# Performance work log

Hardware: AMD Instinct MI355X
Metric: run time of the kernel (lower is better)

Reference implementation:

```python
import jax, jax.numpy as jnp
import numpy as np

N_DIMS = 64
N_HALF = N_DIMS // 2
HIDDEN = 512
N_LAYERS = 8
BATCH = 16384

IDX_EVEN = np.arange(0, N_DIMS, 2)  # mask != 0 for even layers
IDX_ODD = np.arange(1, N_DIMS, 2)


def _init_mlp_params(key, n_in, n_hidden, n_out, n_layers):
    ks = jax.random.split(key, 3)
    def lin(k, fi, fo):
        return jax.random.normal(k, (n_layers, fi, fo), dtype=jnp.float32) / np.sqrt(fi)
    W1 = lin(ks[0], n_in, n_hidden)
    W2 = lin(ks[1], n_hidden, n_hidden)
    W3 = lin(ks[2], n_hidden, n_out)
    b1 = jnp.zeros((n_layers, n_hidden), jnp.float32)
    b2 = jnp.zeros((n_layers, n_hidden), jnp.float32)
    b3 = jnp.zeros((n_layers, n_out), jnp.float32)
    return W1, b1, W2, b2, W3, b3


def setup_inputs() -> dict:
    key = jax.random.key(0)
    ky, kt, ks = jax.random.split(key, 3)
    y = jax.random.normal(ky, (BATCH, N_DIMS), dtype=jnp.float32)
    tW1, tb1, tW2, tb2, tW3, tb3 = _init_mlp_params(kt, N_HALF, HIDDEN, N_HALF, N_LAYERS)
    sW1, sb1, sW2, sb2, sW3, sb3 = _init_mlp_params(ks, N_HALF, HIDDEN, N_HALF, N_LAYERS)
    s_scale = jnp.ones((N_LAYERS, N_HALF), jnp.float32)
    s_shift = jnp.zeros((N_LAYERS, N_HALF), jnp.float32)
    return {
        "y": y,
        "tW1": tW1, "tb1": tb1, "tW2": tW2, "tb2": tb2, "tW3": tW3, "tb3": tb3,
        "sW1": sW1, "sb1": sb1, "sW2": sW2, "sb2": sb2, "sW3": sW3, "sb3": sb3,
        "s_scale": s_scale, "s_shift": s_shift,
    }


def _mlp(x, W1, b1, W2, b2, W3, b3):
    h = jax.nn.relu(x @ W1 + b1)
    h = jax.nn.relu(h @ W2 + b2)
    return h @ W3 + b3


def reference(y, tW1, tb1, tW2, tb2, tW3, tb3,
              sW1, sb1, sW2, sb2, sW3, sb3, s_scale, s_shift):
    z = y
    log_det = jnp.zeros_like(y)
    for i in range(N_LAYERS):
        i0 = IDX_EVEN if i % 2 == 0 else IDX_ODD  # transformed half
        i1 = IDX_ODD if i % 2 == 0 else IDX_EVEN  # conditioning half
        z0 = z[:, i0]  # [B, 32]
        z1 = z[:, i1]  # [B, 32]
        t = _mlp(z1, tW1[i], tb1[i], tW2[i], tb2[i], tW3[i], tb3[i])
        s = jnp.tanh(_mlp(z1, sW1[i], sb1[i], sW2[i], sb2[i], sW3[i], sb3[i])) * s_scale[i] + s_shift[i]
        z0 = z0 * jnp.exp(s) + t
        z = z.at[:, i0].set(z0)
        log_det = log_det.at[:, i0].add(s)
    return z, log_det
```

## Files before the change

kernel.cpp:

```cpp
#include <hip/hip_runtime.h>

typedef unsigned short u16;
typedef unsigned int   u32;
typedef _Float16 f16;
typedef __attribute__((ext_vector_type(8))) _Float16 half8;
typedef __attribute__((ext_vector_type(4))) float f32x4;

#define NBATCH 16384

__device__ __forceinline__ u16 f2h(float x) {
  union { f16 h; u16 u; } v; v.h = (f16)x; return v.u;
}

__global__ __launch_bounds__(256) void cvt_w(
    const float* __restrict__ tsrc, const float* __restrict__ ssrc,
    u16* __restrict__ dst, int M, int N)
{
  __shared__ float tile[32][33];
  int z = blockIdx.z;
  const float* src = ((z & 1) ? ssrc : tsrc) + (size_t)(z >> 1) * M * N;
  u16* d = dst + (size_t)z * M * N;
  int n0 = blockIdx.x * 32, m0 = blockIdx.y * 32;
  for (int r = 0; r < 4; r++) {
    int m = m0 + threadIdx.y + r * 8, n = n0 + threadIdx.x;
    tile[threadIdx.y + r * 8][threadIdx.x] = src[(size_t)m * N + n];
  }
  __syncthreads();
  for (int r = 0; r < 4; r++) {
    int n = n0 + threadIdx.y + r * 8, m = m0 + threadIdx.x;
    d[(size_t)n * M + m] = f2h(tile[threadIdx.x][threadIdx.y + r * 8]);
  }
}

__global__ __launch_bounds__(512, 2) void meganvp(
    const float* __restrict__ y,
    const u16* __restrict__ W1T, const u16* __restrict__ W2T, const u16* __restrict__ W3T,
    const float* __restrict__ tb1, const float* __restrict__ sb1,
    const float* __restrict__ tb2, const float* __restrict__ sb2,
    const float* __restrict__ tb3, const float* __restrict__ sb3,
    const float* __restrict__ s_scale, const float* __restrict__ s_shift,
    float* __restrict__ out)
{
  __shared__ u16 buf[64 * 512];
  __shared__ u16 X[64 * 40];
  __shared__ float TS[64 * 68];

  const int t = threadIdx.x;
  const int m0 = blockIdx.x * 64;
  const int lane = t & 63, w = t >> 6, lm = lane & 15, quad = lane >> 4;
  const int cw = w * 64;
  const int phase = blockIdx.x & 15;
  const int zr = t >> 3, zq = t & 7, c0 = zq * 8;

  float z[8], ld[8];
  {
    const float* yb = y + (size_t)(m0 + zr) * 64 + c0;
    f32x4 v0 = *(const f32x4*)&yb[0];
    f32x4 v1 = *(const f32x4*)&yb[4];
#pragma unroll
    for (int k = 0; k < 4; k++) { z[k] = v0[k]; z[4 + k] = v1[k]; }
#pragma unroll
    for (int e = 0; e < 8; e++) ld[e] = 0.f;
  }

  for (int layer = 0; layer < 8; layer++) {
    const int par = layer & 1;
    {
      union { u16 a[4]; uint2 v; } xv;
#pragma unroll
      for (int e = 0; e < 4; e++) xv.a[e] = f2h(z[2 * e + 1 - par]);
      *(uint2*)&X[zr * 40 + zq * 4] = xv.v;
    }
    __syncthreads();

    for (int net = 0; net < 2; net++) {
      const int idx = layer * 2 + net;

      {
        const float* b1p = (net ? sb1 : tb1) + layer * 512 + cw + lm;
        float bias1[4];
#pragma unroll
        for (int ct = 0; ct < 4; ct++) bias1[ct] = b1p[ct * 16];
        const u16* W1p = W1T + ((size_t)idx * 512 + cw + lm) * 32 + quad * 8;
        half8 bv[4];
#pragma unroll
        for (int ct = 0; ct < 4; ct++) bv[ct] = *(const half8*)&W1p[ct * 512];
        half8 av[4];
#pragma unroll
        for (int rt = 0; rt < 4; rt++)
          av[rt] = *(const half8*)&X[(rt * 16 + lm) * 40 + quad * 8];
        f32x4 zz = {0.f, 0.f, 0.f, 0.f};
        f32x4 acc[4][4];
#pragma unroll
        for (int rt = 0; rt < 4; rt++)
#pragma unroll
          for (int ct = 0; ct < 4; ct++)
            acc[rt][ct] = __builtin_amdgcn_mfma_f32_16x16x32_f16(av[rt], bv[ct], zz, 0, 0, 0);
#pragma unroll
        for (int rt = 0; rt < 4; rt++) {
          const int mrow = rt * 16 + quad * 4;
#pragma unroll
          for (int ct = 0; ct < 4; ct++) {
            const int n = cw + ct * 16 + lm;
#pragma unroll
            for (int r = 0; r < 4; r++) {
              float v = acc[rt][ct][r] + bias1[ct];
              v = v > 0.f ? v : 0.f;
              const int m = mrow + r;
              buf[m * 512 + ((((n >> 3) ^ (m & 7)) << 3) | (n & 7))] = f2h(v);
            }
          }
        }
      }
      __syncthreads();

      {
        const float* b2p = (net ? sb2 : tb2) + layer * 512 + cw + lm;
        float bias2[4];
#pragma unroll
        for (int ct = 0; ct < 4; ct++) bias2[ct] = b2p[ct * 16];
        const u16* W2p = W2T + ((size_t)idx * 512 + cw + lm) * 512 + quad * 8;
        f32x4 zz = {0.f, 0.f, 0.f, 0.f};
        f32x4 acc[4][4];
#pragma unroll
        for (int rt = 0; rt < 4; rt++)
#pragma unroll
          for (int ct = 0; ct < 4; ct++) acc[rt][ct] = zz;
        half8 bb[2][4];
        {
          const int kk0 = (phase & 15) * 32, kk1 = ((phase + 1) & 15) * 32;
#pragma unroll
          for (int ct = 0; ct < 4; ct++) {
            bb[0][ct] = *(const half8*)&W2p[ct * 8192 + kk0];
            bb[1][ct] = *(const half8*)&W2p[ct * 8192 + kk1];
          }
        }
#pragma unroll
        for (int ci = 0; ci < 16; ci++) {
          const int kk = ((ci + phase) & 15) * 32;
          half8 av[4];
#pragma unroll
          for (int rt = 0; rt < 4; rt++) {
            const int m = rt * 16 + lm;
            av[rt] = *(const half8*)&buf[m * 512 + ((((kk >> 3) + quad) ^ (m & 7)) << 3)];
          }
          half8 cur[4];
#pragma unroll
          for (int ct = 0; ct < 4; ct++) cur[ct] = bb[ci & 1][ct];
          if (ci < 14) {
            const int kn = ((ci + 2 + phase) & 15) * 32;
#pragma unroll
            for (int ct = 0; ct < 4; ct++)
              bb[ci & 1][ct] = *(const half8*)&W2p[ct * 8192 + kn];
          }
#pragma unroll
          for (int rt = 0; rt < 4; rt++)
#pragma unroll
            for (int ct = 0; ct < 4; ct++)
              acc[rt][ct] = __builtin_amdgcn_mfma_f32_16x16x32_f16(av[rt], cur[ct], acc[rt][ct], 0, 0, 0);
        }
        __syncthreads();
#pragma unroll
        for (int rt = 0; rt < 4; rt++) {
          const int mrow = rt * 16 + quad * 4;
#pragma unroll
          for (int ct = 0; ct < 4; ct++) {
            const int n = cw + ct * 16 + lm;
#pragma unroll
            for (int r = 0; r < 4; r++) {
              float v = acc[rt][ct][r] + bias2[ct];
              v = v > 0.f ? v : 0.f;
              const int m = mrow + r;
              buf[m * 512 + ((((n >> 3) ^ (m & 7)) << 3) | (n & 7))] = f2h(v);
            }
          }
        }
      }
      __syncthreads();

      {
        const int hr = (w & 3) * 16, hc = (w >> 2) * 16;
        const u16* W3p = W3T + ((size_t)idx * 32 + hc + lm) * 512 + quad * 8;
        f32x4 ha[2];
        ha[0] = (f32x4){0.f, 0.f, 0.f, 0.f}; ha[1] = ha[0];
        const int m = hr + lm;
#pragma unroll
        for (int ci = 0; ci < 16; ci++) {
          const int kk = ((ci + phase) & 15) * 32;
          half8 av = *(const half8*)&buf[m * 512 + ((((kk >> 3) + quad) ^ (m & 7)) << 3)];
          half8 bv = *(const half8*)&W3p[kk];
          ha[ci & 1] = __builtin_amdgcn_mfma_f32_16x16x32_f16(av, bv, ha[ci & 1], 0, 0, 0);
        }
        const int j = hc + lm;
        if (net == 0) {
          const float b3 = tb3[layer * 32 + j];
#pragma unroll
          for (int r = 0; r < 4; r++) {
            const int mm = hr + quad * 4 + r;
            TS[mm * 68 + 2 * j] = ha[0][r] + ha[1][r] + b3;
          }
        } else {
          const int jj = layer * 32 + j;
          const float b3 = sb3[jj], sc = s_scale[jj], sh = s_shift[jj];
#pragma unroll
          for (int r = 0; r < 4; r++) {
            const int mm = hr + quad * 4 + r;
            TS[mm * 68 + 2 * j + 1] = tanhf(ha[0][r] + ha[1][r] + b3) * sc + sh;
          }
        }
      }
      __syncthreads();
    }

    {
      const float* base = &TS[zr * 68 + zq * 8];
      f32x4 q0 = *(const f32x4*)&base[0];
      f32x4 q1 = *(const f32x4*)&base[4];
      float q[8];
#pragma unroll
      for (int k = 0; k < 4; k++) { q[k] = q0[k]; q[4 + k] = q1[k]; }
#pragma unroll
      for (int e = 0; e < 4; e++) {
        const float tv = q[2 * e], sv = q[2 * e + 1];
        const int zi = 2 * e + par;
        z[zi] = z[zi] * expf(sv) + tv;
        ld[zi] += sv;
      }
    }
    __syncthreads();
  }

  {
    float* zb = out + (size_t)(m0 + zr) * 64 + c0;
    float* lb = out + (size_t)NBATCH * 64 + (size_t)(m0 + zr) * 64 + c0;
    f32x4 v0, v1, l0, l1;
#pragma unroll
    for (int k = 0; k < 4; k++) {
      v0[k] = z[k]; v1[k] = z[4 + k];
      l0[k] = ld[k]; l1[k] = ld[4 + k];
    }
    *(f32x4*)&zb[0] = v0; *(f32x4*)&zb[4] = v1;
    *(f32x4*)&lb[0] = l0; *(f32x4*)&lb[4] = l1;
  }
}

extern "C" void kernel_launch(void* const* d_in, const int* in_sizes, int n_in,
                              void* d_out, int out_size, void* d_ws, size_t ws_size,
                              hipStream_t stream) {
  (void)in_sizes; (void)n_in; (void)out_size; (void)ws_size;
  const float* y   = (const float*)d_in[0];
  const float* tW1 = (const float*)d_in[1];
  const float* tb1 = (const float*)d_in[2];
  const float* tW2 = (const float*)d_in[3];
  const float* tb2 = (const float*)d_in[4];
  const float* tW3 = (const float*)d_in[5];
  const float* tb3 = (const float*)d_in[6];
  const float* sW1 = (const float*)d_in[7];
  const float* sb1 = (const float*)d_in[8];
  const float* sW2 = (const float*)d_in[9];
  const float* sb2 = (const float*)d_in[10];
  const float* sW3 = (const float*)d_in[11];
  const float* sb3 = (const float*)d_in[12];
  const float* s_scale = (const float*)d_in[13];
  const float* s_shift = (const float*)d_in[14];
  float* out = (float*)d_out;

  char* ws = (char*)d_ws;
  const size_t W1SZ = (size_t)16 * 512 * 32 * 2;
  const size_t W2SZ = (size_t)16 * 512 * 512 * 2;
  u16* W1 = (u16*)(ws);
  u16* W2 = (u16*)(ws + W1SZ);
  u16* W3 = (u16*)(ws + W1SZ + W2SZ);

  cvt_w<<<dim3(16, 1, 16), dim3(32, 8), 0, stream>>>(tW1, sW1, W1, 32, 512);
  cvt_w<<<dim3(16, 16, 16), dim3(32, 8), 0, stream>>>(tW2, sW2, W2, 512, 512);
  cvt_w<<<dim3(1, 16, 16), dim3(32, 8), 0, stream>>>(tW3, sW3, W3, 512, 32);

  meganvp<<<256, 512, 0, stream>>>(y, W1, W2, W3, tb1, sb1, tb2, sb2, tb3, sb3,
                                   s_scale, s_shift, out);
}
```

Baseline: 469.6 us.

## Double threads per block in coupling kernel and merge weight conversion launches

The fused coupling kernel now runs 1024 threads per block, so 16 waves split each 64-row tile into two 32-row halves while keeping a 64-column slice each. This halves per-wave accumulators and the register load, aiming for more waves in flight to hide MFMA and memory latency on the same 256 blocks. The three weight-conversion kernels are merged into one launch to cut launch overhead, and the trailing barrier after the z update is dropped. Every wave now loads the full W2 column slice for only half the rows, doubling W2 reads per block. Only half the waves work in the W3 stage, and launch_bounds(1024,4) may force tight register limits or spills.

```diff
diff --git a/kernel.cpp b/kernel.cpp
--- a/kernel.cpp
+++ b/kernel.cpp
@@ -12,15 +12,21 @@
   union { f16 h; u16 u; } v; v.h = (f16)x; return v.u;
 }
 
-__global__ __launch_bounds__(256) void cvt_w(
-    const float* __restrict__ tsrc, const float* __restrict__ ssrc,
-    u16* __restrict__ dst, int M, int N)
+__global__ __launch_bounds__(256) void cvt_all(
+    const float* __restrict__ tW1, const float* __restrict__ sW1,
+    const float* __restrict__ tW2, const float* __restrict__ sW2,
+    const float* __restrict__ tW3, const float* __restrict__ sW3,
+    u16* __restrict__ dW1, u16* __restrict__ dW2, u16* __restrict__ dW3)
 {
   __shared__ float tile[32][33];
-  int z = blockIdx.z;
+  const int z = blockIdx.z, bx = blockIdx.x;
+  const float *tsrc, *ssrc; u16* dst; int M, N, nt, mt;
+  if (bx < 16)       { tsrc = tW1; ssrc = sW1; dst = dW1; M = 32;  N = 512; nt = bx;           mt = 0; }
+  else if (bx < 272) { tsrc = tW2; ssrc = sW2; dst = dW2; M = 512; N = 512; nt = (bx - 16) & 15; mt = (bx - 16) >> 4; }
+  else               { tsrc = tW3; ssrc = sW3; dst = dW3; M = 512; N = 32;  nt = 0;            mt = bx - 272; }
   const float* src = ((z & 1) ? ssrc : tsrc) + (size_t)(z >> 1) * M * N;
   u16* d = dst + (size_t)z * M * N;
-  int n0 = blockIdx.x * 32, m0 = blockIdx.y * 32;
+  const int n0 = nt * 32, m0 = mt * 32;
   for (int r = 0; r < 4; r++) {
     int m = m0 + threadIdx.y + r * 8, n = n0 + threadIdx.x;
     tile[threadIdx.y + r * 8][threadIdx.x] = src[(size_t)m * N + n];
@@ -32,7 +38,7 @@
   }
 }
 
-__global__ __launch_bounds__(512, 2) void meganvp(
+__global__ __launch_bounds__(1024, 4) void meganvp(
     const float* __restrict__ y,
     const u16* __restrict__ W1T, const u16* __restrict__ W2T, const u16* __restrict__ W3T,
     const float* __restrict__ tb1, const float* __restrict__ sb1,
@@ -48,28 +54,26 @@
   const int t = threadIdx.x;
   const int m0 = blockIdx.x * 64;
   const int lane = t & 63, w = t >> 6, lm = lane & 15, quad = lane >> 4;
-  const int cw = w * 64;
+  const int r0 = (w & 1) * 32;
+  const int cw = (w >> 1) * 64;
   const int phase = blockIdx.x & 15;
-  const int zr = t >> 3, zq = t & 7, c0 = zq * 8;
-
-  float z[8], ld[8];
+  const int zr = t >> 4, zc0 = (t & 15) * 4;
+
+  float z[4], ld[4];
   {
-    const float* yb = y + (size_t)(m0 + zr) * 64 + c0;
-    f32x4 v0 = *(const f32x4*)&yb[0];
-    f32x4 v1 = *(const f32x4*)&yb[4];
-#pragma unroll
-    for (int k = 0; k < 4; k++) { z[k] = v0[k]; z[4 + k] = v1[k]; }
-#pragma unroll
-    for (int e = 0; e < 8; e++) ld[e] = 0.f;
+    const float* yb = y + (size_t)(m0 + zr) * 64 + zc0;
+    f32x4 v = *(const f32x4*)yb;
+#pragma unroll
+    for (int k = 0; k < 4; k++) { z[k] = v[k]; ld[k] = 0.f; }
   }
 
   for (int layer = 0; layer < 8; layer++) {
     const int par = layer & 1;
     {
-      union { u16 a[4]; uint2 v; } xv;
-#pragma unroll
-      for (int e = 0; e < 4; e++) xv.a[e] = f2h(z[2 * e + 1 - par]);
-      *(uint2*)&X[zr * 40 + zq * 4] = xv.v;
+      union { u16 a[2]; u32 v; } xv;
+      xv.a[0] = f2h(z[1 - par]);
+      xv.a[1] = f2h(z[3 - par]);
+      *(u32*)&X[zr * 40 + (zc0 >> 1)] = xv.v;
     }
     __syncthreads();
 
@@ -85,20 +89,20 @@
         half8 bv[4];
 #pragma unroll
         for (int ct = 0; ct < 4; ct++) bv[ct] = *(const half8*)&W1p[ct * 512];
-        half8 av[4];
-#pragma unroll
-        for (int rt = 0; rt < 4; rt++)
-          av[rt] = *(const half8*)&X[(rt * 16 + lm) * 40 + quad * 8];
+        half8 av[2];
+#pragma unroll
+        for (int rt = 0; rt < 2; rt++)
+          av[rt] = *(const half8*)&X[(r0 + rt * 16 + lm) * 40 + quad * 8];
         f32x4 zz = {0.f, 0.f, 0.f, 0.f};
-        f32x4 acc[4][4];
-#pragma unroll
-        for (int rt = 0; rt < 4; rt++)
+        f32x4 acc[2][4];
+#pragma unroll
+        for (int rt = 0; rt < 2; rt++)
 #pragma unroll
           for (int ct = 0; ct < 4; ct++)
             acc[rt][ct] = __builtin_amdgcn_mfma_f32_16x16x32_f16(av[rt], bv[ct], zz, 0, 0, 0);
 #pragma unroll
-        for (int rt = 0; rt < 4; rt++) {
-          const int mrow = rt * 16 + quad * 4;
+        for (int rt = 0; rt < 2; rt++) {
+          const int mrow = r0 + rt * 16 + quad * 4;
 #pragma unroll
           for (int ct = 0; ct < 4; ct++) {
             const int n = cw + ct * 16 + lm;
@@ -121,9 +125,9 @@
         for (int ct = 0; ct < 4; ct++) bias2[ct] = b2p[ct * 16];
         const u16* W2p = W2T + ((size_t)idx * 512 + cw + lm) * 512 + quad * 8;
         f32x4 zz = {0.f, 0.f, 0.f, 0.f};
-        f32x4 acc[4][4];
-#pragma unroll
-        for (int rt = 0; rt < 4; rt++)
+        f32x4 acc[2][4];
+#pragma unroll
+        for (int rt = 0; rt < 2; rt++)
 #pragma unroll
           for (int ct = 0; ct < 4; ct++) acc[rt][ct] = zz;
         half8 bb[2][4];
@@ -138,10 +142,10 @@
 #pragma unroll
         for (int ci = 0; ci < 16; ci++) {
           const int kk = ((ci + phase) & 15) * 32;
-          half8 av[4];
-#pragma unroll
-          for (int rt = 0; rt < 4; rt++) {
-            const int m = rt * 16 + lm;
+          half8 av[2];
+#pragma unroll
+          for (int rt = 0; rt < 2; rt++) {
+            const int m = r0 + rt * 16 + lm;
             av[rt] = *(const half8*)&buf[m * 512 + ((((kk >> 3) + quad) ^ (m & 7)) << 3)];
           }
           half8 cur[4];
@@ -154,15 +158,15 @@
               bb[ci & 1][ct] = *(const half8*)&W2p[ct * 8192 + kn];
           }
 #pragma unroll
-          for (int rt = 0; rt < 4; rt++)
+          for (int rt = 0; rt < 2; rt++)
 #pragma unroll
             for (int ct = 0; ct < 4; ct++)
               acc[rt][ct] = __builtin_amdgcn_mfma_f32_16x16x32_f16(av[rt], cur[ct], acc[rt][ct], 0, 0, 0);
         }
         __syncthreads();
 #pragma unroll
-        for (int rt = 0; rt < 4; rt++) {
-          const int mrow = rt * 16 + quad * 4;
+        for (int rt = 0; rt < 2; rt++) {
+          const int mrow = r0 + rt * 16 + quad * 4;
 #pragma unroll
           for (int ct = 0; ct < 4; ct++) {
             const int n = cw + ct * 16 + lm;
@@ -178,7 +182,7 @@
       }
       __syncthreads();
 
-      {
+      if (w < 8) {
         const int hr = (w & 3) * 16, hc = (w >> 2) * 16;
         const u16* W3p = W3T + ((size_t)idx * 32 + hc + lm) * 512 + quad * 8;
         f32x4 ha[2];
@@ -213,34 +217,20 @@
     }
 
     {
-      const float* base = &TS[zr * 68 + zq * 8];
-      f32x4 q0 = *(const f32x4*)&base[0];
-      f32x4 q1 = *(const f32x4*)&base[4];
-      float q[8];
-#pragma unroll
-      for (int k = 0; k < 4; k++) { q[k] = q0[k]; q[4 + k] = q1[k]; }
-#pragma unroll
-      for (int e = 0; e < 4; e++) {
-        const float tv = q[2 * e], sv = q[2 * e + 1];
-        const int zi = 2 * e + par;
-        z[zi] = z[zi] * expf(sv) + tv;
-        ld[zi] += sv;
-      }
+      f32x4 q = *(const f32x4*)&TS[zr * 68 + zc0];
+      z[par]     = z[par]     * expf(q[1]) + q[0];  ld[par]     += q[1];
+      z[2 + par] = z[2 + par] * expf(q[3]) + q[2];  ld[2 + par] += q[3];
     }
-    __syncthreads();
   }
 
   {
-    float* zb = out + (size_t)(m0 + zr) * 64 + c0;
-    float* lb = out + (size_t)NBATCH * 64 + (size_t)(m0 + zr) * 64 + c0;
-    f32x4 v0, v1, l0, l1;
-#pragma unroll
-    for (int k = 0; k < 4; k++) {
-      v0[k] = z[k]; v1[k] = z[4 + k];
-      l0[k] = ld[k]; l1[k] = ld[4 + k];
-    }
-    *(f32x4*)&zb[0] = v0; *(f32x4*)&zb[4] = v1;
-    *(f32x4*)&lb[0] = l0; *(f32x4*)&lb[4] = l1;
+    float* zb = out + (size_t)(m0 + zr) * 64 + zc0;
+    float* lb = out + (size_t)NBATCH * 64 + (size_t)(m0 + zr) * 64 + zc0;
+    f32x4 v0, l0;
+#pragma unroll
+    for (int k = 0; k < 4; k++) { v0[k] = z[k]; l0[k] = ld[k]; }
+    *(f32x4*)zb = v0;
+    *(f32x4*)lb = l0;
   }
 }
 
@@ -272,10 +262,9 @@
   u16* W2 = (u16*)(ws + W1SZ);
   u16* W3 = (u16*)(ws + W1SZ + W2SZ);
 
-  cvt_w<<<dim3(16, 1, 16), dim3(32, 8), 0, stream>>>(tW1, sW1, W1, 32, 512);
-  cvt_w<<<dim3(16, 16, 16), dim3(32, 8), 0, stream>>>(tW2, sW2, W2, 512, 512);
-  cvt_w<<<dim3(1, 16, 16), dim3(32, 8), 0, stream>>>(tW3, sW3, W3, 512, 32);
-
-  meganvp<<<256, 512, 0, stream>>>(y, W1, W2, W3, tb1, sb1, tb2, sb2, tb3, sb3,
-                                   s_scale, s_shift, out);
-}
+  cvt_all<<<dim3(288, 1, 16), dim3(32, 8), 0, stream>>>(tW1, sW1, tW2, sW2, tW3, sW3,
+                                                        W1, W2, W3);
+
+  meganvp<<<256, 1024, 0, stream>>>(y, W1, W2, W3, tb1, sb1, tb2, sb2, tb3, sb3,
+                                    s_scale, s_shift, out);
+}
```

Result: slower. 694.3 us (+47.9%).
